# Kernel tuning notes

Hardware: AMD Instinct MI355X
Metric: run time of the kernel (lower is better)

The kernel has to match this reference:

```python
import jax, jax.numpy as jnp
import numpy as np

E = 1024      # emb_size == hidden_size
H = 8         # n_heads
BATCH = 8
NUM = 48      # table rows
KW = 48       # table columns (keys)
L = NUM * KW  # 2304


def _mha(q_in, kv_in, length, Wq, bq, Wk, bk, Wv, bv, Wo, bo, n_heads=H):
    # q_in: (B, T, E), kv_in: (B, S, E); returns (T, B, E) per the torch layout.
    B, T, Em = q_in.shape
    S = kv_in.shape[1]
    dh = Em // n_heads
    q = (q_in @ Wq + bq).reshape(B, T, n_heads, dh).transpose(0, 2, 1, 3)
    k = (kv_in @ Wk + bk).reshape(B, S, n_heads, dh).transpose(0, 2, 1, 3)
    v = (kv_in @ Wv + bv).reshape(B, S, n_heads, dh).transpose(0, 2, 1, 3)
    scores = jnp.einsum('bhtd,bhsd->bhts', q, k) / jnp.asarray(np.sqrt(dh), q.dtype)
    mask = jnp.arange(S) < length  # memory_lengths masking
    scores = jnp.where(mask[None, None, None, :], scores, jnp.finfo(scores.dtype).min)
    attn = jax.nn.softmax(scores, axis=-1)
    out = jnp.einsum('bhts,bhsd->bhtd', attn, v).transpose(0, 2, 1, 3).reshape(B, T, Em)
    out = out @ Wo + bo
    return out.transpose(1, 0, 2)  # (T, B, E)


def setup_inputs() -> dict:
    key = jax.random.key(0)
    ks = jax.random.split(key, 24)

    def W(k, shape, s=0.03):
        return jax.random.normal(k, shape, dtype=jnp.float32) * s

    inp = {
        'emb': jax.random.normal(ks[0], (L, BATCH, E), dtype=jnp.float32),
        # col attention params
        'Wq_c': W(ks[1], (E, E)), 'bq_c': jnp.zeros((E,), jnp.float32),
        'Wk_c': W(ks[2], (E, E)), 'bk_c': jnp.zeros((E,), jnp.float32),
        'Wv_c': W(ks[3], (E, E)), 'bv_c': jnp.zeros((E,), jnp.float32),
        'Wo_c': W(ks[4], (E, E)), 'bo_c': jnp.zeros((E,), jnp.float32),
        # row attention params
        'Wq_r': W(ks[5], (E, E)), 'bq_r': jnp.zeros((E,), jnp.float32),
        'Wk_r': W(ks[6], (E, E)), 'bk_r': jnp.zeros((E,), jnp.float32),
        'Wv_r': W(ks[7], (E, E)), 'bv_r': jnp.zeros((E,), jnp.float32),
        'Wo_r': W(ks[8], (E, E)), 'bo_r': jnp.zeros((E,), jnp.float32),
        # fusion layers
        'W_gen': W(ks[9], (2 * E, E)),
        'W_mlp1': W(ks[10], (2 * E, E)),
        'W_mlp2': W(ks[11], (E, 1)),
        # scalar forward args
        'start_id': 0, 'end_id': L - 1,
        'num': NUM, 'num_tensor': NUM,
        'kw_num': KW, 'kw_num_tensor': KW,
        'batch': BATCH,
    }
    return inp


def reference(emb, Wq_c, bq_c, Wk_c, bk_c, Wv_c, bv_c, Wo_c, bo_c,
              Wq_r, bq_r, Wk_r, bk_r, Wv_r, bv_r, Wo_r, bo_r,
              W_gen, W_mlp1, W_mlp2,
              start_id, end_id, num, num_tensor, kw_num, kw_num_tensor, batch):
    Em = emb.shape[-1]
    length = end_id - start_id + 1  # = num * kw_num
    # emb.narrow(0, start_id, length): (L, batch, E)
    rep = emb[start_id:start_id + length]
    # -> (kw_num, batch*num, E)
    home_ply_rep = rep.transpose(1, 0, 2).reshape(batch * num, kw_num, Em).transpose(1, 0, 2)

    # --- column-dim encoding: attention over the `num` (row) axis ---
    col_mb = jnp.swapaxes(home_ply_rep.reshape(kw_num, batch, num, Em), 0, 2)  # (num, batch, kw, E)
    col_mb = col_mb.reshape(num, batch * kw_num, Em)
    col_q = col_mb.transpose(1, 0, 2)  # (batch*kw, num, E)
    col_rep = _mha(col_q, col_q, num_tensor, Wq_c, bq_c, Wk_c, bk_c, Wv_c, bv_c, Wo_c, bo_c)
    # (num, batch*kw, E) -> (kw_num, batch*num, E)
    col_dim_rep = jnp.swapaxes(col_rep.reshape(num, batch, kw_num, Em), 0, 2).reshape(kw_num, batch * num, Em)

    # --- row-dim encoding: attention over the `kw_num` (column) axis ---
    row_q = col_dim_rep.transpose(1, 0, 2)  # (batch*num, kw, E)
    row_dim_rep = _mha(row_q, row_q, kw_num_tensor, Wq_r, bq_r, Wk_r, bk_r, Wv_r, bv_r, Wo_r, bo_r)  # (kw, b*n, E)

    # --- fusion: concat + Linear + tanh, MLP scores, softmax over {row, col} ---
    gen_rep = jnp.tanh(jnp.concatenate([row_dim_rep, col_dim_rep], axis=-1) @ W_gen)

    def mlp_score(x):
        return jnp.tanh(jnp.concatenate([x, gen_rep], axis=-1) @ W_mlp1) @ W_mlp2  # (kw, b*n, 1)

    row_score = mlp_score(row_dim_rep)
    col_score = mlp_score(col_dim_rep)
    w = jax.nn.softmax(jnp.concatenate([row_score, col_score], axis=-1), axis=-1)  # (kw, b*n, 2)
    home_ply_memory_bank = w[..., 0:1] * row_dim_rep + w[..., 1:2] * col_dim_rep
    # no_fusion=True -> residual add
    home_ply_memory_bank = home_ply_memory_bank + home_ply_rep

    row_for_ptr = row_dim_rep.reshape(kw_num, batch, num, Em)
    col_for_ptr = col_dim_rep.reshape(kw_num, batch, num, Em)

    # row_aggregation == 'mean'
    home_ply_row_rep = home_ply_memory_bank.mean(axis=0)  # (batch*num, E)
    home_ply_row_rep = home_ply_row_rep.reshape(batch, num, Em).transpose(1, 0, 2)  # (num, batch, E)
    return (home_ply_row_rep, home_ply_memory_bank, col_for_ptr, row_for_ptr)
```

## Files before the change

### kernel.cpp

```cpp
#include <hip/hip_runtime.h>
#include <hip/hip_bf16.h>
#include <stdint.h>

typedef unsigned short u16;
typedef unsigned int   u32;
typedef __attribute__((ext_vector_type(4))) float f32x4;
typedef __attribute__((ext_vector_type(2))) float f32x2;
typedef __attribute__((ext_vector_type(8))) short s16x8;

#define DEV __device__ __forceinline__

static constexpr int EDIM  = 1024;
static constexpr int MROWS = 8 * 48 * 48;

DEV float b2f(u16 x) { u32 u = ((u32)x) << 16; float f; __builtin_memcpy(&f, &u, 4); return f; }
DEV u16 f2b(float f) {
    u32 u; __builtin_memcpy(&u, &f, 4);
    u32 r = (u + 0x7FFFu + ((u >> 16) & 1u)) >> 16;
    return (u16)r;
}

#define GLDS16(gsrc, ldst) __builtin_amdgcn_global_load_lds( \
    (const __attribute__((address_space(1))) u32*)(gsrc),    \
    (__attribute__((address_space(3))) u32*)(ldst), 16, 0, 0)

enum { F_WRC = 1, F_PERM = 2, F_TANH = 4, F_SCORE = 8, F_OMAP1 = 16, F_OMAP2 = 32,
       F_OUTFLIN = 64, F_HGEN = 128 };

struct GJob {
    const u16* A1; const u16* A2; const u16* Bt; const float* bias;
    u16* C; float* outF; const float* w2; float* score;
    int ldc, M, flags, tileEnd;
};
struct GSet3 { int njobs, pad; GJob j[3]; };

struct WJob { const float* src; u16* dst; int srcN, dstLd, kOff, nT, tileEnd, pad; };
struct WSet { int n, total; WJob j[12]; };

__global__ void wconvJ_kernel(WSet ws) {
    int bid = blockIdx.x;
    int ji = 0;
    while (bid >= ws.j[ji].tileEnd) ++ji;
    int base = ji ? ws.j[ji - 1].tileEnd : 0;
    WJob J = ws.j[ji];
    int lt = bid - base;
    int n0 = (lt % J.nT) * 64, k0 = (lt / J.nT) * 64;
    __shared__ u16 tile[64][65];
    int tx = threadIdx.x & 63, ty = threadIdx.x >> 6;
#pragma unroll
    for (int i = 0; i < 16; ++i) {
        int r = ty * 16 + i;
        tile[r][tx] = f2b(J.src[(size_t)(k0 + r) * J.srcN + n0 + tx]);
    }
    __syncthreads();
#pragma unroll
    for (int i = 0; i < 16; ++i) {
        int r = ty * 16 + i;
        J.dst[(size_t)(n0 + r) * J.dstLd + J.kOff + k0 + tx] = tile[tx][r];
    }
}

__global__ void misc_kernel(const float* WoCsrc, const float* WoRsrc,
                            u16* WoCnt, u16* WoRnt,
                            const float* bq_c, const float* bk_c, const float* bv_c, float* bqkvC,
                            const float* bq_r, const float* bk_r, const float* bv_r,
                            const float* bo_c, const u16* WqkvRT, float* bqkvR_eff,
                            const float* bo_r, const u16* WgaT, float* bgen_lin,
                            float* scores) {
    int id = blockIdx.x * 256 + threadIdx.x;
    const int C1 = 1024 * 1024 / 2;
    if (id < C1) {
        f32x2 v = *(const f32x2*)&WoCsrc[(size_t)id * 2];
        *(u32*)&WoCnt[(size_t)id * 2] = (u32)f2b(v.x) | ((u32)f2b(v.y) << 16);
        return;
    }
    id -= C1;
    if (id < C1) {
        f32x2 v = *(const f32x2*)&WoRsrc[(size_t)id * 2];
        *(u32*)&WoRnt[(size_t)id * 2] = (u32)f2b(v.x) | ((u32)f2b(v.y) << 16);
        return;
    }
    id -= C1;
    if (id < 3072) { bqkvC[id] = (id < 1024) ? bq_c[id] : (id < 2048) ? bk_c[id - 1024] : bv_c[id - 2048]; return; }
    id -= 3072;
    if (id < 2 * MROWS) { scores[id] = 0.f; return; }
    id -= 2 * MROWS;
    if (id < 3072) {
        float s = (id < 1024) ? bq_r[id] : (id < 2048) ? bk_r[id - 1024] : bv_r[id - 2048];
        float d = 0.f;
        const u16* row = &WqkvRT[(size_t)id * 1024];
        for (int e = 0; e < 1024; e += 8) {
            s16x8 v = *(const s16x8*)&row[e];
#pragma unroll
            for (int u = 0; u < 8; ++u) d += bo_c[e + u] * b2f((u16)v[u]);
        }
        bqkvR_eff[id] = s + d;
        return;
    }
    id -= 3072;
    if (id < 1024) {
        float d = 0.f;
        const u16* row = &WgaT[(size_t)id * 1024];
        for (int e = 0; e < 1024; e += 8) {
            s16x8 v = *(const s16x8*)&row[e];
#pragma unroll
            for (int u = 0; u < 8; ++u) d += bo_r[e + u] * b2f((u16)v[u]);
        }
        bgen_lin[id] = d;
    }
}

__global__ void gather_kernel(const float* __restrict__ emb, u16* __restrict__ Xc) {
    int gid = blockIdx.x * 256 + threadIdx.x;
    int r = gid >> 9, c2 = gid & 511;
    int b = r / 2304, k = (r / 48) % 48, n = r % 48;
    int src = (n * 48 + k) * 8 + b;
    f32x2 v = *(const f32x2*)&emb[(size_t)src * EDIM + c2 * 2];
    *(u32*)&Xc[(size_t)r * EDIM + c2 * 2] = (u32)f2b(v.x) | ((u32)f2b(v.y) << 16);
}

template<int LDA, int KT, bool DUAL, int LDA2>
DEV void gemm_core(const GJob& J, int lt) {
    extern __shared__ u16 smem[];
    u16* lA = smem;
    u16* lB = smem + 12288;
    constexpr int NT = KT / 32;

    int mtl = J.M >> 7;
    int mt = lt % mtl, nt = lt / mtl;
    int m0 = mt * 128, n0 = nt * 128;
    int tid = threadIdx.x, lane = tid & 63, wv = tid >> 6;
    int wm = wv >> 1, wn = wv & 1;
    int fr = lane & 15, qq = lane >> 4;

    int c0 = wv * 2, c1 = c0 + 1;
    int r0 = c0 * 16 + (lane >> 2), r1 = c1 * 16 + (lane >> 2);
    int qg0 = ((lane & 3) - (r0 >> 1)) & 3, qg1 = ((lane & 3) - (r1 >> 1)) & 3;
    const u16* gA0 = J.A1 + (size_t)(m0 + r0) * LDA + qg0 * 8;
    const u16* gA1 = J.A1 + (size_t)(m0 + r1) * LDA + qg1 * 8;
    const u16* gA0b = nullptr; const u16* gA1b = nullptr;
    if constexpr (DUAL) {
        gA0b = J.A2 + (size_t)(m0 + r0) * LDA2 + qg0 * 8;
        gA1b = J.A2 + (size_t)(m0 + r1) * LDA2 + qg1 * 8;
    }
    const u16* gB0 = J.Bt + (size_t)(n0 + r0) * KT + qg0 * 8;
    const u16* gB1 = J.Bt + (size_t)(n0 + r1) * KT + qg1 * 8;
    u16* dA0 = lA + c0 * 512;
    u16* dA1 = lA + c1 * 512;
    u16* dB0 = lB + c0 * 512;
    u16* dB1 = lB + c1 * 512;

    const u16* aP[4]; const u16* bP[4];
#pragma unroll
    for (int mf = 0; mf < 4; ++mf) {
        int rr = wm * 64 + mf * 16 + fr;
        aP[mf] = lA + rr * 32 + (((qq + (rr >> 1)) & 3) * 8);
        int rn = wn * 64 + mf * 16 + fr;
        bP[mf] = lB + rn * 32 + (((qq + (rn >> 1)) & 3) * 8);
    }

    f32x4 acc[4][4];
#pragma unroll
    for (int i = 0; i < 4; ++i)
#pragma unroll
        for (int jj = 0; jj < 4; ++jj) acc[i][jj] = (f32x4)0.f;

    auto STAGE = [&](int bsel, int kt) {
        int bo = bsel * 4096;
        if (DUAL && kt >= 32) {
            GLDS16(gA0b + (kt - 32) * 32, dA0 + bo);
            GLDS16(gA1b + (kt - 32) * 32, dA1 + bo);
        } else {
            GLDS16(gA0 + kt * 32, dA0 + bo);
            GLDS16(gA1 + kt * 32, dA1 + bo);
        }
        GLDS16(gB0 + kt * 32, dB0 + bo);
        GLDS16(gB1 + kt * 32, dB1 + bo);
    };

    STAGE(0, 0);
    STAGE(1, 1);
#pragma unroll
    for (int kt = 0; kt < NT; ++kt) {
        if (kt + 1 < NT) asm volatile("s_waitcnt vmcnt(4)" ::: "memory");
        else             asm volatile("s_waitcnt vmcnt(0)" ::: "memory");
        __builtin_amdgcn_s_barrier();
        __builtin_amdgcn_sched_barrier(0);
        if (kt + 2 < NT) STAGE((kt + 2) % 3, kt + 2);
        const int po = (kt % 3) * 4096;
        s16x8 af[4], bf[4];
#pragma unroll
        for (int mf = 0; mf < 4; ++mf) af[mf] = *(const s16x8*)(aP[mf] + po);
#pragma unroll
        for (int nf = 0; nf < 4; ++nf) bf[nf] = *(const s16x8*)(bP[nf] + po);
#pragma unroll
        for (int mf = 0; mf < 4; ++mf)
#pragma unroll
            for (int nf = 0; nf < 4; ++nf)
                acc[mf][nf] = __builtin_amdgcn_mfma_f32_16x16x32_bf16(af[mf], bf[nf], acc[mf][nf], 0, 0, 0);
    }

    int crow4 = qq * 4;
#pragma unroll
    for (int mf = 0; mf < 4; ++mf) {
#pragma unroll
        for (int jj = 0; jj < 4; ++jj) {
            int row = m0 + wm * 64 + mf * 16 + crow4 + jj;
            int orow = row, o32 = 0;
            if (J.flags & (F_PERM | F_OMAP1)) {
                int b = row / 2304, k = (row / 48) % 48, n = row % 48;
                if (J.flags & F_PERM)  orow = (b * 48 + n) * 48 + k;
                if (J.flags & F_OMAP1) o32 = k * 384 + b * 48 + n;
            }
            if (J.flags & F_OMAP2) {
                int b = row / 2304, n = (row / 48) % 48, k = row % 48;
                o32 = k * 384 + b * 48 + n;
            }
            float sc = 0.f;
#pragma unroll
            for (int nf = 0; nf < 4; ++nf) {
                int col = n0 + wn * 64 + nf * 16 + fr;
                float v = acc[mf][nf][jj];
                if (J.bias) v += J.bias[col];
                if (J.flags & F_HGEN) v += J.outF[(size_t)row * EDIM + col];
                if (J.flags & F_TANH) v = tanhf(v);
                if (J.flags & F_WRC) J.C[(size_t)orow * J.ldc + col] = f2b(v);
                if (J.flags & (F_OMAP1 | F_OMAP2)) J.outF[(size_t)o32 * EDIM + col] = v;
                if (J.flags & F_OUTFLIN) J.outF[(size_t)row * EDIM + col] = v;
                if (J.flags & F_SCORE) sc += v * J.w2[col];
            }
            if (J.flags & F_SCORE) {
                sc += __shfl_xor(sc, 1);
                sc += __shfl_xor(sc, 2);
                sc += __shfl_xor(sc, 4);
                sc += __shfl_xor(sc, 8);
                if (fr == 0) atomicAdd(&J.score[row], sc);
            }
        }
    }
}

template<int LDA, int KT, bool DUAL, int LDA2>
__global__ __launch_bounds__(256, 3) void gemmT_kernel(GSet3 js) {
    int bid = blockIdx.x;
    int ji = 0, base = 0;
    if (js.njobs > 1 && bid >= js.j[0].tileEnd) { ji = 1; base = js.j[0].tileEnd; }
    if (js.njobs > 2 && bid >= js.j[1].tileEnd) { ji = 2; base = js.j[1].tileEnd; }
    gemm_core<LDA, KT, DUAL, LDA2>(js.j[ji], bid - base);
}

__global__ __launch_bounds__(256, 3) void gemmD3_kernel(GJob a, GJob b, int aTiles) {
    int bid = blockIdx.x;
    if (bid < aTiles) gemm_core<1024, 1024, false, 0>(a, bid);
    else              gemm_core<1024, 2048, true, 1024>(b, bid - aTiles);
}

__global__ __launch_bounds__(64) void attn_kernel(const u16* __restrict__ QKV,
                                                  u16* __restrict__ O) {
    __shared__ u16 lVt[128 * 72];
    __shared__ u16 lP[48 * 72];
    const int LDQ = 3072;
    int bb = blockIdx.x >> 3, h = blockIdx.x & 7;
    int lane = threadIdx.x;
    const u16* Qp = QKV + (size_t)bb * 48 * LDQ + h * 128;
    const u16* Kp = Qp + 1024;
    const u16* Vp = Qp + 2048;
    u16* Op = O + (size_t)bb * 48 * 1024 + h * 128;

#pragma unroll
    for (int i = 0; i < 48; ++i) {
        u32 vv = *(const u32*)&Vp[(size_t)i * LDQ + lane * 2];
        lVt[(lane * 2) * 72 + i]     = (u16)(vv & 0xffffu);
        lVt[(lane * 2 + 1) * 72 + i] = (u16)(vv >> 16);
    }
    for (int i = lane; i < 128 * 16; i += 64) { int d = i >> 4, c = 48 + (i & 15); lVt[d * 72 + c] = 0; }
    for (int i = lane; i < 48 * 16; i += 64)  { int t = i >> 4, c = 48 + (i & 15); lP[t * 72 + c] = 0; }
    __syncthreads();

    int fr = lane & 15, fk = (lane >> 4) * 8, crow4 = (lane >> 4) * 4;
    f32x4 sc[3][3];
#pragma unroll
    for (int mf = 0; mf < 3; ++mf)
#pragma unroll
        for (int nf = 0; nf < 3; ++nf) sc[mf][nf] = (f32x4)0.f;

#pragma unroll
    for (int kk = 0; kk < 4; ++kk) {
        s16x8 aq[3], bk[3];
#pragma unroll
        for (int mf = 0; mf < 3; ++mf) aq[mf] = *(const s16x8*)&Qp[(size_t)(mf * 16 + fr) * LDQ + kk * 32 + fk];
#pragma unroll
        for (int nf = 0; nf < 3; ++nf) bk[nf] = *(const s16x8*)&Kp[(size_t)(nf * 16 + fr) * LDQ + kk * 32 + fk];
#pragma unroll
        for (int mf = 0; mf < 3; ++mf)
#pragma unroll
            for (int nf = 0; nf < 3; ++nf)
                sc[mf][nf] = __builtin_amdgcn_mfma_f32_16x16x32_bf16(aq[mf], bk[nf], sc[mf][nf], 0, 0, 0);
    }

    const float scale = 0.08838834764831845f;
#pragma unroll
    for (int mf = 0; mf < 3; ++mf) {
#pragma unroll
        for (int j = 0; j < 4; ++j) {
            float v0 = sc[mf][0][j] * scale;
            float v1 = sc[mf][1][j] * scale;
            float v2 = sc[mf][2][j] * scale;
            float mx = fmaxf(v0, fmaxf(v1, v2));
            mx = fmaxf(mx, __shfl_xor(mx, 1));
            mx = fmaxf(mx, __shfl_xor(mx, 2));
            mx = fmaxf(mx, __shfl_xor(mx, 4));
            mx = fmaxf(mx, __shfl_xor(mx, 8));
            float e0 = __expf(v0 - mx), e1 = __expf(v1 - mx), e2 = __expf(v2 - mx);
            float s = e0 + e1 + e2;
            s += __shfl_xor(s, 1);
            s += __shfl_xor(s, 2);
            s += __shfl_xor(s, 4);
            s += __shfl_xor(s, 8);
            float inv = 1.f / s;
            int t = mf * 16 + crow4 + j;
            lP[t * 72 + 0  + fr] = f2b(e0 * inv);
            lP[t * 72 + 16 + fr] = f2b(e1 * inv);
            lP[t * 72 + 32 + fr] = f2b(e2 * inv);
        }
    }
    __syncthreads();

    f32x4 o[3][8];
#pragma unroll
    for (int mf = 0; mf < 3; ++mf)
#pragma unroll
        for (int nf = 0; nf < 8; ++nf) o[mf][nf] = (f32x4)0.f;

#pragma unroll
    for (int kk = 0; kk < 2; ++kk) {
        s16x8 ap[3];
#pragma unroll
        for (int mf = 0; mf < 3; ++mf) ap[mf] = *(const s16x8*)&lP[(mf * 16 + fr) * 72 + kk * 32 + fk];
#pragma unroll
        for (int nf = 0; nf < 8; ++nf) {
            s16x8 bv = *(const s16x8*)&lVt[(nf * 16 + fr) * 72 + kk * 32 + fk];
#pragma unroll
            for (int mf = 0; mf < 3; ++mf)
                o[mf][nf] = __builtin_amdgcn_mfma_f32_16x16x32_bf16(ap[mf], bv, o[mf][nf], 0, 0, 0);
        }
    }
#pragma unroll
    for (int mf = 0; mf < 3; ++mf)
#pragma unroll
        for (int nf = 0; nf < 8; ++nf)
#pragma unroll
            for (int j = 0; j < 4; ++j) {
                int t = mf * 16 + crow4 + j, d = nf * 16 + fr;
                Op[(size_t)t * 1024 + d] = f2b(o[mf][nf][j]);
            }
}

__global__ void combine_mean_kernel(const u16* __restrict__ RDR, const u16* __restrict__ CDR,
                                    const float* __restrict__ srow, const float* __restrict__ scol,
                                    const float* __restrict__ emb, float* __restrict__ out) {
    int b = blockIdx.x / 48, n = blockIdx.x % 48;
    __shared__ float w0s[48], w1s[48];
    int tx = threadIdx.x;
    if (tx < 48) {
        int r2 = (b * 48 + n) * 48 + tx;
        float rs = srow[r2], cs = scol[r2];
        float m = fmaxf(rs, cs);
        float e0 = __expf(rs - m), e1 = __expf(cs - m);
        float inv = 1.f / (e0 + e1);
        w0s[tx] = e0 * inv; w1s[tx] = e1 * inv;
    }
    __syncthreads();
    float* out_mb = out + 393216;
    for (int e = tx; e < EDIM; e += 256) {
        float s = 0.f;
        for (int k = 0; k < 48; ++k) {
            size_t rb = (size_t)((b * 48 + n) * 48 + k) * EDIM;
            float rv = b2f(RDR[rb + e]);
            float cv = b2f(CDR[rb + e]);
            float hv = emb[((size_t)(n * 48 + k) * 8 + b) * EDIM + e];
            float v = w0s[k] * rv + w1s[k] * cv + hv;
            out_mb[(size_t)(k * 384 + b * 48 + n) * EDIM + e] = v;
            s += v;
        }
        out[(size_t)(n * 8 + b) * EDIM + e] = s * (1.f / 48.f);
    }
}

extern "C" void kernel_launch(void* const* d_in, const int* in_sizes, int n_in,
                              void* d_out, int out_size, void* d_ws, size_t ws_size,
                              hipStream_t stream) {
    const float* emb    = (const float*)d_in[0];
    const float* Wq_c   = (const float*)d_in[1];
    const float* bq_c   = (const float*)d_in[2];
    const float* Wk_c   = (const float*)d_in[3];
    const float* bk_c   = (const float*)d_in[4];
    const float* Wv_c   = (const float*)d_in[5];
    const float* bv_c   = (const float*)d_in[6];
    const float* Wo_c   = (const float*)d_in[7];
    const float* bo_c   = (const float*)d_in[8];
    const float* Wq_r   = (const float*)d_in[9];
    const float* bq_r   = (const float*)d_in[10];
    const float* Wk_r   = (const float*)d_in[11];
    const float* bk_r   = (const float*)d_in[12];
    const float* Wv_r   = (const float*)d_in[13];
    const float* bv_r   = (const float*)d_in[14];
    const float* Wo_r   = (const float*)d_in[15];
    const float* bo_r   = (const float*)d_in[16];
    const float* W_gen  = (const float*)d_in[17];
    const float* W_mlp1 = (const float*)d_in[18];
    const float* W_mlp2 = (const float*)d_in[19];
    (void)in_sizes; (void)n_in; (void)out_size; (void)ws_size;

    char* ws = (char*)d_ws;
    size_t off = 0;
    auto alloc = [&](size_t bytes) { char* p = ws + off; off += (bytes + 255) & ~(size_t)255; return p; };
    u16*   WqkvCT = (u16*)alloc((size_t)3072 * 1024 * 2);
    u16*   WqkvRT = (u16*)alloc((size_t)3072 * 1024 * 2);
    u16*   WoCT   = (u16*)alloc((size_t)1024 * 1024 * 2);
    u16*   WoRT   = (u16*)alloc((size_t)1024 * 1024 * 2);
    u16*   WoCnt  = (u16*)alloc((size_t)1024 * 1024 * 2);
    u16*   WoRnt  = (u16*)alloc((size_t)1024 * 1024 * 2);
    u16*   WgaT   = (u16*)alloc((size_t)1024 * 1024 * 2);
    u16*   BtGf   = (u16*)alloc((size_t)1024 * 2048 * 2);
    u16*   W1aT   = (u16*)alloc((size_t)1024 * 1024 * 2);
    u16*   W1bT   = (u16*)alloc((size_t)1024 * 1024 * 2);
    u16*   BtQKVr = (u16*)alloc((size_t)3072 * 1024 * 2);
    float* bqkvC  = (float*)alloc(3072 * 4);
    float* bqkvRe = (float*)alloc(3072 * 4);
    float* bgen   = (float*)alloc(1024 * 4);
    u16*   XA     = (u16*)alloc((size_t)MROWS * 1024 * 2);
    u16*   XO     = (u16*)alloc((size_t)MROWS * 1024 * 2);
    u16*   QKV    = (u16*)alloc((size_t)MROWS * 3072 * 2);
    u16*   QKV2   = (u16*)alloc((size_t)MROWS * 3072 * 2);
    u16*   CDR    = (u16*)alloc((size_t)MROWS * 1024 * 2);
    u16*   RDR    = (u16*)alloc((size_t)MROWS * 1024 * 2);
    float* score_row = (float*)alloc((size_t)MROWS * 4);
    float* score_col = (float*)alloc((size_t)MROWS * 4);
    float* Hgen = (float*)QKV;

    float* out = (float*)d_out;
    float* out_col = out + 393216 + 18874368;
    float* out_row = out + 393216 + 2 * 18874368;

    dim3 tb(256);
    const int SMEM = 49152;

    WSet wset = {};
    int te = 0;
    auto addW = [&](const float* src, u16* dst, int srcN, int dstLd, int kOff, int nT, int kT) {
        int i = wset.n++;
        te += nT * kT;
        WJob w = {src, dst, srcN, dstLd, kOff, nT, te, 0};
        wset.j[i] = w;
    };
    addW(Wq_c, WqkvCT,                   1024, 1024, 0, 16, 16);
    addW(Wk_c, WqkvCT + 1024 * 1024,     1024, 1024, 0, 16, 16);
    addW(Wv_c, WqkvCT + 2 * 1024 * 1024, 1024, 1024, 0, 16, 16);
    addW(Wo_c, WoCT,                     1024, 1024, 0, 16, 16);
    addW(Wq_r, WqkvRT,                   1024, 1024, 0, 16, 16);
    addW(Wk_r, WqkvRT + 1024 * 1024,     1024, 1024, 0, 16, 16);
    addW(Wv_r, WqkvRT + 2 * 1024 * 1024, 1024, 1024, 0, 16, 16);
    addW(Wo_r, WoRT,                     1024, 1024, 0, 16, 16);
    addW(W_gen,               WgaT,      1024, 1024, 0, 16, 16);
    addW(W_gen + 1024 * 1024, BtGf,      1024, 2048, 1024, 16, 16);
    addW(W_mlp1,               W1aT,     1024, 1024, 0, 16, 16);
    addW(W_mlp1 + 1024 * 1024, W1bT,     1024, 1024, 0, 16, 16);
    wset.total = te;
    wconvJ_kernel<<<te, tb, 0, stream>>>(wset);

    int miscItems = 1024 * 1024 + 3072 + 2 * MROWS + 3072 + 1024;
    misc_kernel<<<(miscItems + 255) / 256, tb, 0, stream>>>(
        Wo_c, Wo_r, WoCnt, WoRnt,
        bq_c, bk_c, bv_c, bqkvC,
        bq_r, bk_r, bv_r,
        bo_c, WqkvRT, bqkvRe,
        bo_r, WgaT, bgen,
        score_row);

    gather_kernel<<<MROWS * 512 / 256, tb, 0, stream>>>(emb, XA);

    auto mkJob = [](const u16* A1, const u16* A2, const u16* Bt, const float* bias,
                    u16* C, float* outF, const float* w2, float* score,
                    int ldc, int M, int flags) {
        GJob j = {A1, A2, Bt, bias, C, outF, w2, score, ldc, M, flags, 0};
        return j;
    };
    auto mkset = [](GJob a, int nA, const GJob* b, int nB, const GJob* c, int nC, int& tot) {
        GSet3 gs = {};
        a.tileEnd = (a.M >> 7) * nA;
        gs.j[0] = a; tot = a.tileEnd; gs.njobs = 1;
        if (b) { GJob jb = *b; jb.tileEnd = tot + (jb.M >> 7) * nB; tot = jb.tileEnd; gs.j[1] = jb; gs.njobs = 2; }
        if (c) { GJob jc = *c; jc.tileEnd = tot + (jc.M >> 7) * nC; tot = jc.tileEnd; gs.j[2] = jc; gs.njobs = 3; }
        return gs;
    };

    {
        GJob b = mkJob(WqkvRT, nullptr, WoCnt, nullptr, BtQKVr, nullptr, nullptr, nullptr,
                       1024, 3072, F_WRC);
        GJob c = mkJob(WgaT, nullptr, WoRnt, nullptr, BtGf, nullptr, nullptr, nullptr,
                       2048, 1024, F_WRC);
        int tot;
        GSet3 gs = mkset(mkJob(XA, nullptr, WqkvCT, bqkvC, QKV, nullptr, nullptr, nullptr,
                               3072, MROWS, F_WRC), 24, &b, 8, &c, 8, tot);
        gemmT_kernel<1024, 1024, false, 0><<<tot, tb, SMEM, stream>>>(gs);
    }
    attn_kernel<<<384 * 8, 64, 0, stream>>>(QKV, XO);
    {
        GJob b = mkJob(XO, nullptr, BtQKVr, bqkvRe, QKV2, nullptr, nullptr, nullptr,
                       3072, MROWS, F_WRC | F_PERM);
        int tot;
        GSet3 gs = mkset(mkJob(XO, nullptr, WoCT, bo_c, CDR, out_col, nullptr, nullptr,
                               1024, MROWS, F_WRC | F_PERM | F_OMAP1), 8, &b, 24, nullptr, 0, tot);
        gemmT_kernel<1024, 1024, false, 0><<<tot, tb, SMEM, stream>>>(gs);
    }
    attn_kernel<<<384 * 8, 64, 0, stream>>>(QKV2, XO);
    {
        GJob a = mkJob(XO, nullptr, WoRT, bo_r, RDR, out_row, nullptr, nullptr,
                       1024, MROWS, F_WRC | F_OMAP2);
        GJob b = mkJob(XO, CDR, BtGf, bgen, XA, nullptr, nullptr, nullptr,
                       1024, MROWS, F_WRC | F_TANH);
        int aT = (MROWS >> 7) * 8;
        int bT = (MROWS >> 7) * 8;
        gemmD3_kernel<<<aT + bT, tb, SMEM, stream>>>(a, b, aT);
    }
    {
        int tot;
        GSet3 gs = mkset(mkJob(XA, nullptr, W1bT, nullptr, nullptr, Hgen, nullptr, nullptr,
                               1024, MROWS, F_OUTFLIN), 8, nullptr, 0, nullptr, 0, tot);
        gemmT_kernel<1024, 1024, false, 0><<<tot, tb, SMEM, stream>>>(gs);
    }
    {
        GJob b = mkJob(CDR, nullptr, W1aT, nullptr, nullptr, Hgen, W_mlp2, score_col,
                       1024, MROWS, F_SCORE | F_TANH | F_HGEN);
        int tot;
        GSet3 gs = mkset(mkJob(RDR, nullptr, W1aT, nullptr, nullptr, Hgen, W_mlp2, score_row,
                               1024, MROWS, F_SCORE | F_TANH | F_HGEN), 8, &b, 8, nullptr, 0, tot);
        gemmT_kernel<1024, 1024, false, 0><<<tot, tb, SMEM, stream>>>(gs);
    }

    combine_mean_kernel<<<384, tb, 0, stream>>>(RDR, CDR, score_row, score_col, emb, out);
}
```

Baseline: 1.168 ms.

## Enlarge GEMM tile to 256x128 with double-buffered LDS pipeline

```diff
diff --git a/kernel.cpp b/kernel.cpp
--- a/kernel.cpp
+++ b/kernel.cpp
@@ -123,78 +123,83 @@
 DEV void gemm_core(const GJob& J, int lt) {
     extern __shared__ u16 smem[];
     u16* lA = smem;
-    u16* lB = smem + 12288;
+    u16* lB = smem + 16384;
     constexpr int NT = KT / 32;
 
-    int mtl = J.M >> 7;
+    int mtl = J.M >> 8;
     int mt = lt % mtl, nt = lt / mtl;
-    int m0 = mt * 128, n0 = nt * 128;
+    int m0 = mt * 256, n0 = nt * 128;
     int tid = threadIdx.x, lane = tid & 63, wv = tid >> 6;
     int wm = wv >> 1, wn = wv & 1;
     int fr = lane & 15, qq = lane >> 4;
 
-    int c0 = wv * 2, c1 = c0 + 1;
-    int r0 = c0 * 16 + (lane >> 2), r1 = c1 * 16 + (lane >> 2);
-    int qg0 = ((lane & 3) - (r0 >> 1)) & 3, qg1 = ((lane & 3) - (r1 >> 1)) & 3;
-    const u16* gA0 = J.A1 + (size_t)(m0 + r0) * LDA + qg0 * 8;
-    const u16* gA1 = J.A1 + (size_t)(m0 + r1) * LDA + qg1 * 8;
-    const u16* gA0b = nullptr; const u16* gA1b = nullptr;
-    if constexpr (DUAL) {
-        gA0b = J.A2 + (size_t)(m0 + r0) * LDA2 + qg0 * 8;
-        gA1b = J.A2 + (size_t)(m0 + r1) * LDA2 + qg1 * 8;
-    }
-    const u16* gB0 = J.Bt + (size_t)(n0 + r0) * KT + qg0 * 8;
-    const u16* gB1 = J.Bt + (size_t)(n0 + r1) * KT + qg1 * 8;
-    u16* dA0 = lA + c0 * 512;
-    u16* dA1 = lA + c1 * 512;
-    u16* dB0 = lB + c0 * 512;
-    u16* dB1 = lB + c1 * 512;
-
-    const u16* aP[4]; const u16* bP[4];
-#pragma unroll
-    for (int mf = 0; mf < 4; ++mf) {
-        int rr = wm * 64 + mf * 16 + fr;
+    const u16* gA[4]; const u16* gAb[4]; u16* dA[4];
+    const u16* gB[2]; u16* dB[2];
+    int lrow = lane >> 2;
+    int lg = lane & 3;
+#pragma unroll
+    for (int i = 0; i < 4; ++i) {
+        int c = wv * 4 + i;
+        int rr = c * 16 + lrow;
+        int qg = (lg - (rr >> 1)) & 3;
+        gA[i] = J.A1 + (size_t)(m0 + rr) * LDA + qg * 8;
+        if constexpr (DUAL) gAb[i] = J.A2 + (size_t)(m0 + rr) * LDA2 + qg * 8;
+        dA[i] = lA + c * 512;
+    }
+#pragma unroll
+    for (int i = 0; i < 2; ++i) {
+        int c = wv * 2 + i;
+        int rr = c * 16 + lrow;
+        int qg = (lg - (rr >> 1)) & 3;
+        gB[i] = J.Bt + (size_t)(n0 + rr) * KT + qg * 8;
+        dB[i] = lB + c * 512;
+    }
+
+    const u16* aP[8]; const u16* bP[4];
+#pragma unroll
+    for (int mf = 0; mf < 8; ++mf) {
+        int rr = wm * 128 + mf * 16 + fr;
         aP[mf] = lA + rr * 32 + (((qq + (rr >> 1)) & 3) * 8);
-        int rn = wn * 64 + mf * 16 + fr;
-        bP[mf] = lB + rn * 32 + (((qq + (rn >> 1)) & 3) * 8);
-    }
-
-    f32x4 acc[4][4];
-#pragma unroll
-    for (int i = 0; i < 4; ++i)
+    }
+#pragma unroll
+    for (int nf = 0; nf < 4; ++nf) {
+        int rn = wn * 64 + nf * 16 + fr;
+        bP[nf] = lB + rn * 32 + (((qq + (rn >> 1)) & 3) * 8);
+    }
+
+    f32x4 acc[8][4];
+#pragma unroll
+    for (int i = 0; i < 8; ++i)
 #pragma unroll
         for (int jj = 0; jj < 4; ++jj) acc[i][jj] = (f32x4)0.f;
 
     auto STAGE = [&](int bsel, int kt) {
-        int bo = bsel * 4096;
+        int boA = bsel * 8192, boB = bsel * 4096;
         if (DUAL && kt >= 32) {
-            GLDS16(gA0b + (kt - 32) * 32, dA0 + bo);
-            GLDS16(gA1b + (kt - 32) * 32, dA1 + bo);
+#pragma unroll
+            for (int i = 0; i < 4; ++i) GLDS16(gAb[i] + (kt - 32) * 32, dA[i] + boA);
         } else {
-            GLDS16(gA0 + kt * 32, dA0 + bo);
-            GLDS16(gA1 + kt * 32, dA1 + bo);
-        }
-        GLDS16(gB0 + kt * 32, dB0 + bo);
-        GLDS16(gB1 + kt * 32, dB1 + bo);
+#pragma unroll
+            for (int i = 0; i < 4; ++i) GLDS16(gA[i] + kt * 32, dA[i] + boA);
+        }
+#pragma unroll
+        for (int i = 0; i < 2; ++i) GLDS16(gB[i] + kt * 32, dB[i] + boB);
     };
 
     STAGE(0, 0);
-    STAGE(1, 1);
 #pragma unroll
     for (int kt = 0; kt < NT; ++kt) {
-        if (kt + 1 < NT) asm volatile("s_waitcnt vmcnt(4)" ::: "memory");
-        else             asm volatile("s_waitcnt vmcnt(0)" ::: "memory");
-        __builtin_amdgcn_s_barrier();
-        __builtin_amdgcn_sched_barrier(0);
-        if (kt + 2 < NT) STAGE((kt + 2) % 3, kt + 2);
-        const int po = (kt % 3) * 4096;
-        s16x8 af[4], bf[4];
-#pragma unroll
-        for (int mf = 0; mf < 4; ++mf) af[mf] = *(const s16x8*)(aP[mf] + po);
-#pragma unroll
-        for (int nf = 0; nf < 4; ++nf) bf[nf] = *(const s16x8*)(bP[nf] + po);
-#pragma unroll
-        for (int mf = 0; mf < 4; ++mf)
+        __syncthreads();
+        if (kt + 1 < NT) STAGE((kt + 1) & 1, kt + 1);
+        const int poA = (kt & 1) * 8192;
+        const int poB = (kt & 1) * 4096;
+        s16x8 af[8], bf[4];
+#pragma unroll
+        for (int mf = 0; mf < 8; ++mf) af[mf] = *(const s16x8*)(aP[mf] + poA);
+#pragma unroll
+        for (int nf = 0; nf < 4; ++nf) bf[nf] = *(const s16x8*)(bP[nf] + poB);
+#pragma unroll
+        for (int mf = 0; mf < 8; ++mf)
 #pragma unroll
             for (int nf = 0; nf < 4; ++nf)
                 acc[mf][nf] = __builtin_amdgcn_mfma_f32_16x16x32_bf16(af[mf], bf[nf], acc[mf][nf], 0, 0, 0);
@@ -202,10 +207,10 @@
 
     int crow4 = qq * 4;
 #pragma unroll
-    for (int mf = 0; mf < 4; ++mf) {
+    for (int mf = 0; mf < 8; ++mf) {
 #pragma unroll
         for (int jj = 0; jj < 4; ++jj) {
-            int row = m0 + wm * 64 + mf * 16 + crow4 + jj;
+            int row = m0 + wm * 128 + mf * 16 + crow4 + jj;
             int orow = row, o32 = 0;
             if (J.flags & (F_PERM | F_OMAP1)) {
                 int b = row / 2304, k = (row / 48) % 48, n = row % 48;
@@ -241,7 +246,7 @@
 }
 
 template<int LDA, int KT, bool DUAL, int LDA2>
-__global__ __launch_bounds__(256, 3) void gemmT_kernel(GSet3 js) {
+__global__ __launch_bounds__(256, 2) void gemmT_kernel(GSet3 js) {
     int bid = blockIdx.x;
     int ji = 0, base = 0;
     if (js.njobs > 1 && bid >= js.j[0].tileEnd) { ji = 1; base = js.j[0].tileEnd; }
@@ -249,7 +254,7 @@
     gemm_core<LDA, KT, DUAL, LDA2>(js.j[ji], bid - base);
 }
 
-__global__ __launch_bounds__(256, 3) void gemmD3_kernel(GJob a, GJob b, int aTiles) {
+__global__ __launch_bounds__(256, 2) void gemmD3_kernel(GJob a, GJob b, int aTiles) {
     int bid = blockIdx.x;
     if (bid < aTiles) gemm_core<1024, 1024, false, 0>(a, bid);
     else              gemm_core<1024, 2048, true, 1024>(b, bid - aTiles);
@@ -488,10 +493,10 @@
     };
     auto mkset = [](GJob a, int nA, const GJob* b, int nB, const GJob* c, int nC, int& tot) {
         GSet3 gs = {};
-        a.tileEnd = (a.M >> 7) * nA;
+        a.tileEnd = (a.M >> 8) * nA;
         gs.j[0] = a; tot = a.tileEnd; gs.njobs = 1;
-        if (b) { GJob jb = *b; jb.tileEnd = tot + (jb.M >> 7) * nB; tot = jb.tileEnd; gs.j[1] = jb; gs.njobs = 2; }
-        if (c) { GJob jc = *c; jc.tileEnd = tot + (jc.M >> 7) * nC; tot = jc.tileEnd; gs.j[2] = jc; gs.njobs = 3; }
+        if (b) { GJob jb = *b; jb.tileEnd = tot + (jb.M >> 8) * nB; tot = jb.tileEnd; gs.j[1] = jb; gs.njobs = 2; }
+        if (c) { GJob jc = *c; jc.tileEnd = tot + (jc.M >> 8) * nC; tot = jc.tileEnd; gs.j[2] = jc; gs.njobs = 3; }
         return gs;
     };
 
@@ -520,8 +525,8 @@
                        1024, MROWS, F_WRC | F_OMAP2);
         GJob b = mkJob(XO, CDR, BtGf, bgen, XA, nullptr, nullptr, nullptr,
                        1024, MROWS, F_WRC | F_TANH);
-        int aT = (MROWS >> 7) * 8;
-        int bT = (MROWS >> 7) * 8;
+        int aT = (MROWS >> 8) * 8;
+        int bT = (MROWS >> 8) * 8;
         gemmD3_kernel<<<aT + bT, tb, SMEM, stream>>>(a, b, aT);
     }
     {
```

Measured after the change: 1.492 ms. +27.8%, slower.
